# Kernel optimization log

Hardware: AMD Instinct MI355X
Metric: run time of the kernel (lower is better)

The kernel has to match this reference:

```python
import jax, jax.numpy as jnp
import numpy as np


def setup_inputs() -> dict:
    key = jax.random.key(0)
    ks = jax.random.split(key, 8)
    B, E = 1024, 8
    dims = [480, 512, 512, 311]
    inp = {
        "x": jax.random.normal(ks[0], (B, dims[0]), dtype=jnp.float32),
        "weight_blend": jax.random.uniform(ks[1], (E, B), dtype=jnp.float32),
        "w0": jax.random.normal(ks[2], (E, dims[1], dims[0]), dtype=jnp.float32) * 0.05,
        "b0": jax.random.normal(ks[3], (E, dims[1]), dtype=jnp.float32) * 0.05,
        "w1": jax.random.normal(ks[4], (E, dims[2], dims[1]), dtype=jnp.float32) * 0.05,
        "b1": jax.random.normal(ks[5], (E, dims[2]), dtype=jnp.float32) * 0.05,
        "w2": jax.random.normal(ks[6], (E, dims[3], dims[2]), dtype=jnp.float32) * 0.05,
        "b2": jax.random.normal(ks[7], (E, dims[3]), dtype=jnp.float32) * 0.05,
    }
    return inp


def _blend_layer(h, blend, w, b):
    # Original: W_b = sum_e blend[e,b] * w[e]  (materializes [B, d_out, d_in]),
    # then matmul(W_b, h) + bias_b. Fused einsum computes identical math.
    out = jnp.einsum("eb,eoi,bi->bo", blend, w, h)
    out = out + jnp.einsum("eb,eo->bo", blend, b)
    return out


def reference(x, weight_blend, w0, b0, w1, b1, w2, b2):
    # dropout layers are identity (training=False / keep_prob=1)
    h = _blend_layer(x, weight_blend, w0, b0)
    h = jax.nn.elu(h)
    h = _blend_layer(h, weight_blend, w1, b1)
    h = jax.nn.elu(h)
    h = _blend_layer(h, weight_blend, w2, b2)  # no activation on final layer
    return h
```

## Files before the change

### kernel.cpp

```cpp
#include <hip/hip_runtime.h>

typedef __attribute__((ext_vector_type(8))) short short8;
typedef __attribute__((ext_vector_type(4))) float f32x4;

__device__ __forceinline__ unsigned short f2bf(float f) {
    unsigned u = __builtin_bit_cast(unsigned, f);
    unsigned r = (u + 0x7FFFu + ((u >> 16) & 1u)) >> 16;
    return (unsigned short)r;
}
__device__ __forceinline__ float bf2f(unsigned short u) {
    unsigned v = ((unsigned)u) << 16;
    return __builtin_bit_cast(float, v);
}

__device__ __forceinline__ void gload16(const unsigned short* g, unsigned short* l) {
    __builtin_amdgcn_global_load_lds(
        (const __attribute__((address_space(1))) void*)g,
        (__attribute__((address_space(3))) void*)l,
        16, 0, 0);
}

#define WAITV(N) asm volatile("s_waitcnt vmcnt(" #N ")" ::: "memory")
#define WAITL0() asm volatile("s_waitcnt lgkmcnt(0)" ::: "memory")
#define BAR() do { asm volatile("" ::: "memory"); __builtin_amdgcn_s_barrier(); asm volatile("" ::: "memory"); } while (0)

__device__ __forceinline__ short8 lds_read_swz(const unsigned short* tile, int row, int colb) {
    int off = row * 64 + colb;
    off ^= ((off >> 7) & 7) << 4;
    return *(const short8*)((const char*)tile + off);
}

__device__ __forceinline__ void xcd_decode(int bid, int nxt, int& x, int& y, int& z) {
    int r = bid & 7, q = bid >> 3;
    y = q & 7;
    int p = (q >> 3) * 8 + r;
    x = p % nxt; z = p / nxt;
}

__device__ __forceinline__ void cvt_chunk(const float* __restrict__ src,
                                          unsigned short* __restrict__ dst, int t) {
    const float4* s4 = (const float4*)src;
    float4 a = s4[2 * t], b = s4[2 * t + 1];
    union { unsigned short u[8]; int4 v; } r;
    r.u[0] = f2bf(a.x); r.u[1] = f2bf(a.y); r.u[2] = f2bf(a.z); r.u[3] = f2bf(a.w);
    r.u[4] = f2bf(b.x); r.u[5] = f2bf(b.y); r.u[6] = f2bf(b.z); r.u[7] = f2bf(b.w);
    ((int4*)dst)[t] = r.v;
}

__device__ __forceinline__ short8 pack8(float4 a, float4 b) {
    short8 p;
    p[0] = (short)f2bf(a.x); p[1] = (short)f2bf(a.y);
    p[2] = (short)f2bf(a.z); p[3] = (short)f2bf(a.w);
    p[4] = (short)f2bf(b.x); p[5] = (short)f2bf(b.y);
    p[6] = (short)f2bf(b.z); p[7] = (short)f2bf(b.w);
    return p;
}

__global__ __launch_bounds__(512) void k_gemm0(
    const float* __restrict__ A, const float* __restrict__ W,
    const float* __restrict__ blend, const float* __restrict__ bias,
    unsigned short* __restrict__ Y,
    const float* __restrict__ csrc, unsigned short* __restrict__ cdst)
{
    __shared__ unsigned short As[2][4096];
    __shared__ unsigned short Bs[2][4096];

    int bx, by, e;
    xcd_decode(blockIdx.x, 4, bx, by, e);
    const int bm = by * 128;
    const int on = bx * 128;
    const int t  = threadIdx.x, lane = t & 63, w = t >> 6;
    const int wr = w >> 2, wc = w & 3;

    const int sr = lane >> 2, sce = (lane & 3) * 8;
    const int ra = w * 16 + sr;
    const float* gA = A + (size_t)(bm + ra) * 480 + sce;
    const float* gB = W + ((size_t)e * 512 + (on + ra)) * 480 + sce;

    int woff = ra * 64 + (lane & 3) * 16;
    woff ^= ((woff >> 7) & 7) << 4;

    float4 La0[3], La1[3], Lb0[3], Lb1[3];
    #pragma unroll
    for (int s = 0; s < 3; ++s) {
        int k0 = s * 32;
        La0[s] = *(const float4*)(gA + k0); La1[s] = *(const float4*)(gA + k0 + 4);
        Lb0[s] = *(const float4*)(gB + k0); Lb1[s] = *(const float4*)(gB + k0 + 4);
    }

    f32x4 acc[4][2] = {};

    #pragma unroll
    for (int kt = 0; kt < 15; ++kt) {
        const int s = kt % 3, buf = kt & 1;
        *(short8*)((char*)As[buf] + woff) = pack8(La0[s], La1[s]);
        *(short8*)((char*)Bs[buf] + woff) = pack8(Lb0[s], Lb1[s]);
        WAITL0();
        BAR();
        if (kt + 3 < 15) {
            int k0 = (kt + 3) * 32;
            La0[s] = *(const float4*)(gA + k0); La1[s] = *(const float4*)(gA + k0 + 4);
            Lb0[s] = *(const float4*)(gB + k0); Lb1[s] = *(const float4*)(gB + k0 + 4);
        }
        short8 af[4], bfr[2];
        #pragma unroll
        for (int fm = 0; fm < 4; ++fm)
            af[fm] = lds_read_swz(As[buf], wr * 64 + fm * 16 + (lane & 15), (lane >> 4) * 16);
        #pragma unroll
        for (int fn = 0; fn < 2; ++fn)
            bfr[fn] = lds_read_swz(Bs[buf], wc * 32 + fn * 16 + (lane & 15), (lane >> 4) * 16);
        #pragma unroll
        for (int fm = 0; fm < 4; ++fm)
            #pragma unroll
            for (int fn = 0; fn < 2; ++fn)
                acc[fm][fn] = __builtin_amdgcn_mfma_f32_16x16x32_bf16(
                    af[fm], bfr[fn], acc[fm][fn], 0, 0, 0);
    }

    const float* blendE = blend + e * 1024;
    const float* biasE  = bias + (size_t)e * 512;
    unsigned short* Ye  = Y + (size_t)e * 1024 * 512;
    #pragma unroll
    for (int fm = 0; fm < 4; ++fm) {
        int i0 = bm + wr * 64 + fm * 16 + (lane >> 4) * 4;
        float4 bl = *(const float4*)&blendE[i0];
        #pragma unroll
        for (int fn = 0; fn < 2; ++fn) {
            int j = on + wc * 32 + fn * 16 + (lane & 15);
            float bs = biasE[j];
            #pragma unroll
            for (int r = 0; r < 4; ++r)
                Ye[(size_t)(i0 + r) * 512 + j] = f2bf((acc[fm][fn][r] + bs) * ((&bl.x)[r]));
        }
    }

    int lb = (e * 8 + by) * 4 + bx;
    cvt_chunk(csrc, cdst, lb * 1024 + threadIdx.x);
    cvt_chunk(csrc, cdst, lb * 1024 + 512 + threadIdx.x);
}

__global__ __launch_bounds__(512) void k_gemm(
    const unsigned short* __restrict__ A,
    const unsigned short* __restrict__ W,
    const float* __restrict__ blend, const float* __restrict__ bias,
    unsigned short* __restrict__ Y,
    int N, int ldy, int nxt,
    const float* __restrict__ csrc, unsigned short* __restrict__ cdst, int nchunk)
{
    __shared__ unsigned short As[4][4096];
    __shared__ unsigned short Bs[4][4096];

    int bx, by, e;
    xcd_decode(blockIdx.x, nxt, bx, by, e);
    const int bm = by * 128;
    const int on = bx * 128;
    const int t  = threadIdx.x, lane = t & 63, w = t >> 6;
    const int wr = w >> 2, wc = w & 3;

    const unsigned short* Wt = W + (size_t)e * N * 512;
    const int l2 = lane ^ ((lane >> 3) & 7);
    const int sr = l2 >> 2, sce = (l2 & 3) * 8;
    const int ra = w * 16 + sr;
    int rb = on + ra; if (rb > N - 1) rb = N - 1;
    const unsigned short* gA = A  + (size_t)(bm + ra) * 512 + sce;
    const unsigned short* gB = Wt + (size_t)rb * 512 + sce;

#define STAGE(buf, kt) do { int _k0 = (kt) * 32;                       \
        gload16(gA + _k0, &As[(buf)][w * 512]);                        \
        gload16(gB + _k0, &Bs[(buf)][w * 512]); } while (0)

#define COMPUTE(cur) do {                                                          \
        short8 af[4], bfr[2];                                                      \
        _Pragma("unroll")                                                          \
        for (int fm = 0; fm < 4; ++fm)                                             \
            af[fm] = lds_read_swz(As[(cur)], wr * 64 + fm * 16 + (lane & 15), (lane >> 4) * 16); \
        _Pragma("unroll")                                                          \
        for (int fn = 0; fn < 2; ++fn)                                             \
            bfr[fn] = lds_read_swz(Bs[(cur)], wc * 32 + fn * 16 + (lane & 15), (lane >> 4) * 16); \
        _Pragma("unroll")                                                          \
        for (int fm = 0; fm < 4; ++fm)                                             \
            _Pragma("unroll")                                                      \
            for (int fn = 0; fn < 2; ++fn)                                         \
                acc[fm][fn] = __builtin_amdgcn_mfma_f32_16x16x32_bf16(             \
                    af[fm], bfr[fn], acc[fm][fn], 0, 0, 0);                        \
    } while (0)

    f32x4 acc[4][2] = {};
    STAGE(0, 0); STAGE(1, 1); STAGE(2, 2);

    for (int kt = 0; kt < 13; ++kt) {
        WAITV(4);
        BAR();
        STAGE((kt + 3) & 3, kt + 3);
        COMPUTE(kt & 3);
    }
    WAITV(4); BAR(); COMPUTE(1);
    WAITV(2); BAR(); COMPUTE(2);
    WAITV(0); BAR(); COMPUTE(3);
#undef STAGE

    const float* blendE = blend + e * 1024;
    const float* biasE  = bias + (size_t)e * N;
    unsigned short* Ye  = Y + (size_t)e * 1024 * ldy;
    #pragma unroll
    for (int fm = 0; fm < 4; ++fm) {
        int i0 = bm + wr * 64 + fm * 16 + (lane >> 4) * 4;
        float4 bl = *(const float4*)&blendE[i0];
        #pragma unroll
        for (int fn = 0; fn < 2; ++fn) {
            int j = on + wc * 32 + fn * 16 + (lane & 15);
            if (j < N) {
                float bs = biasE[j];
                #pragma unroll
                for (int r = 0; r < 4; ++r)
                    Ye[(size_t)(i0 + r) * ldy + j] = f2bf((acc[fm][fn][r] + bs) * ((&bl.x)[r]));
            }
        }
    }

    if (cdst) {
        int lb = (e * 8 + by) * nxt + bx;
        #pragma unroll
        for (int q = 0; q < 2; ++q) {
            int tl = q * 512 + threadIdx.x;
            if (tl < nchunk) cvt_chunk(csrc, cdst, lb * nchunk + tl);
        }
    }
}

__global__ __launch_bounds__(256) void k_reduce8(
    const unsigned short* __restrict__ Y, unsigned short* __restrict__ out)
{
    int idx = blockIdx.x * 256 + threadIdx.x;
    int b  = idx >> 6;
    int o0 = (idx & 63) * 8;
    size_t base = (size_t)b * 512 + o0;
    float s[8] = {};
    #pragma unroll
    for (int p = 0; p < 8; ++p) {
        int4 v = *(const int4*)&Y[base + (size_t)p * 1024 * 512];
        const unsigned short* u = (const unsigned short*)&v;
        #pragma unroll
        for (int r = 0; r < 8; ++r) s[r] += bf2f(u[r]);
    }
    union { unsigned short u[8]; int4 v; } rr;
    #pragma unroll
    for (int r = 0; r < 8; ++r) {
        float v = (s[r] > 0.f) ? s[r] : expm1f(s[r]);
        rr.u[r] = f2bf(v);
    }
    *(int4*)&out[base] = rr.v;
}

__global__ __launch_bounds__(256) void k_reduce_last(
    const unsigned short* __restrict__ Y, float* __restrict__ out)
{
    int idx = blockIdx.x * 256 + threadIdx.x;
    if (idx >= 1024 * 40) return;
    int b  = idx / 40;
    int o0 = (idx - b * 40) * 8;
    size_t base = (size_t)b * 320 + o0;
    float s[8] = {};
    #pragma unroll
    for (int p = 0; p < 8; ++p) {
        int4 v = *(const int4*)&Y[base + (size_t)p * 1024 * 320];
        const unsigned short* u = (const unsigned short*)&v;
        #pragma unroll
        for (int r = 0; r < 8; ++r) s[r] += bf2f(u[r]);
    }
    #pragma unroll
    for (int r = 0; r < 8; ++r)
        if (o0 + r < 311) out[(size_t)b * 311 + o0 + r] = s[r];
}

extern "C" void kernel_launch(void* const* d_in, const int* in_sizes, int n_in,
                              void* d_out, int out_size, void* d_ws, size_t ws_size,
                              hipStream_t stream) {
    const float* x     = (const float*)d_in[0];
    const float* blend = (const float*)d_in[1];
    const float* w0    = (const float*)d_in[2];
    const float* b0    = (const float*)d_in[3];
    const float* w1    = (const float*)d_in[4];
    const float* b1    = (const float*)d_in[5];
    const float* w2    = (const float*)d_in[6];
    const float* b2    = (const float*)d_in[7];

    char* ws = (char*)d_ws;
    unsigned short* w1b = (unsigned short*)(ws + 0);
    unsigned short* w2b = (unsigned short*)(ws + 4194304);
    unsigned short* h1b = (unsigned short*)(ws + 6742016);
    unsigned short* h2b = (unsigned short*)(ws + 7790592);
    unsigned short* yb  = (unsigned short*)(ws + 8839168);

    k_gemm0<<<256, 512, 0, stream>>>(x, w0, blend, b0, yb, w1, w1b);
    k_reduce8<<<256, 256, 0, stream>>>(yb, h1b);

    k_gemm<<<256, 512, 0, stream>>>(h1b, w1b, blend, b1, yb, 512, 512, 4,
                                    w2, w2b, 622);
    k_reduce8<<<256, 256, 0, stream>>>(yb, h2b);

    k_gemm<<<192, 512, 0, stream>>>(h2b, w2b, blend, b2, yb, 311, 320, 3,
                                    nullptr, nullptr, 0);
    k_reduce_last<<<160, 256, 0, stream>>>(yb, (float*)d_out);
}
```

Measured before the change: 53.17 us.

## Split K across two warp groups with LDS reduction in blended GEMM

The 8 waves are split into two groups that process alternating K tiles. Each wave now computes a 64x64 output subtile (4x4 MFMA fragments) instead of 64x32, which halves the LDS fragment reads per MFMA. The partial accumulators are then reduced through shared memory in two rounds before one group writes the epilogue. This doubles the accumulator registers per wave and adds extra barriers and LDS traffic for the reduction.

Result: slower. 59.48 us (+11.9%).

```diff
diff --git a/kernel.cpp b/kernel.cpp
--- a/kernel.cpp
+++ b/kernel.cpp
@@ -147,15 +147,18 @@
     int N, int ldy, int nxt,
     const float* __restrict__ csrc, unsigned short* __restrict__ cdst, int nchunk)
 {
-    __shared__ unsigned short As[4][4096];
-    __shared__ unsigned short Bs[4][4096];
+    __shared__ char smem[65536];
+    unsigned short (*As)[4096] = (unsigned short (*)[4096])smem;
+    unsigned short (*Bs)[4096] = (unsigned short (*)[4096])(smem + 32768);
 
     int bx, by, e;
     xcd_decode(blockIdx.x, nxt, bx, by, e);
     const int bm = by * 128;
     const int on = bx * 128;
     const int t  = threadIdx.x, lane = t & 63, w = t >> 6;
-    const int wr = w >> 2, wc = w & 3;
+    const int wk = w >> 2;
+    const int ws = w & 3;
+    const int wr = ws >> 1, wc = ws & 1;
 
     const unsigned short* Wt = W + (size_t)e * N * 512;
     const int l2 = lane ^ ((lane >> 3) & 7);
@@ -170,50 +173,86 @@
         gload16(gB + _k0, &Bs[(buf)][w * 512]); } while (0)
 
 #define COMPUTE(cur) do {                                                          \
-        short8 af[4], bfr[2];                                                      \
+        short8 af[4], bfr[4];                                                      \
         _Pragma("unroll")                                                          \
         for (int fm = 0; fm < 4; ++fm)                                             \
             af[fm] = lds_read_swz(As[(cur)], wr * 64 + fm * 16 + (lane & 15), (lane >> 4) * 16); \
         _Pragma("unroll")                                                          \
-        for (int fn = 0; fn < 2; ++fn)                                             \
-            bfr[fn] = lds_read_swz(Bs[(cur)], wc * 32 + fn * 16 + (lane & 15), (lane >> 4) * 16); \
+        for (int fn = 0; fn < 4; ++fn)                                             \
+            bfr[fn] = lds_read_swz(Bs[(cur)], wc * 64 + fn * 16 + (lane & 15), (lane >> 4) * 16); \
         _Pragma("unroll")                                                          \
         for (int fm = 0; fm < 4; ++fm)                                             \
             _Pragma("unroll")                                                      \
-            for (int fn = 0; fn < 2; ++fn)                                         \
+            for (int fn = 0; fn < 4; ++fn)                                         \
                 acc[fm][fn] = __builtin_amdgcn_mfma_f32_16x16x32_bf16(             \
                     af[fm], bfr[fn], acc[fm][fn], 0, 0, 0);                        \
     } while (0)
 
-    f32x4 acc[4][2] = {};
+    f32x4 acc[4][4] = {};
     STAGE(0, 0); STAGE(1, 1); STAGE(2, 2);
 
     for (int kt = 0; kt < 13; ++kt) {
         WAITV(4);
         BAR();
         STAGE((kt + 3) & 3, kt + 3);
-        COMPUTE(kt & 3);
-    }
-    WAITV(4); BAR(); COMPUTE(1);
-    WAITV(2); BAR(); COMPUTE(2);
-    WAITV(0); BAR(); COMPUTE(3);
+        if ((kt & 1) == wk) COMPUTE(kt & 3);
+    }
+    WAITV(4); BAR(); if (wk == 1) COMPUTE(1);
+    WAITV(2); BAR(); if (wk == 0) COMPUTE(2);
+    WAITV(0); BAR(); if (wk == 1) COMPUTE(3);
 #undef STAGE
 
-    const float* blendE = blend + e * 1024;
-    const float* biasE  = bias + (size_t)e * N;
-    unsigned short* Ye  = Y + (size_t)e * 1024 * ldy;
-    #pragma unroll
-    for (int fm = 0; fm < 4; ++fm) {
-        int i0 = bm + wr * 64 + fm * 16 + (lane >> 4) * 4;
-        float4 bl = *(const float4*)&blendE[i0];
-        #pragma unroll
-        for (int fn = 0; fn < 2; ++fn) {
-            int j = on + wc * 32 + fn * 16 + (lane & 15);
-            if (j < N) {
-                float bs = biasE[j];
+    float* fsc = (float*)smem;
+    #pragma unroll
+    for (int rnd = 0; rnd < 2; ++rnd) {
+        BAR();
+        if (wk == 1 && (ws >> 1) == rnd) {
+            float* base = fsc + (ws & 1) * 4096;
+            #pragma unroll
+            for (int fm = 0; fm < 4; ++fm)
                 #pragma unroll
-                for (int r = 0; r < 4; ++r)
-                    Ye[(size_t)(i0 + r) * ldy + j] = f2bf((acc[fm][fn][r] + bs) * ((&bl.x)[r]));
+                for (int fn = 0; fn < 4; ++fn)
+                    #pragma unroll
+                    for (int r = 0; r < 4; ++r) {
+                        int row = fm * 16 + (lane >> 4) * 4 + r;
+                        int col = fn * 16 + (lane & 15);
+                        base[row * 64 + col] = acc[fm][fn][r];
+                    }
+        }
+        WAITL0();
+        BAR();
+        if (wk == 0 && (ws >> 1) == rnd) {
+            float* base = fsc + (ws & 1) * 4096;
+            #pragma unroll
+            for (int fm = 0; fm < 4; ++fm)
+                #pragma unroll
+                for (int fn = 0; fn < 4; ++fn)
+                    #pragma unroll
+                    for (int r = 0; r < 4; ++r) {
+                        int row = fm * 16 + (lane >> 4) * 4 + r;
+                        int col = fn * 16 + (lane & 15);
+                        acc[fm][fn][r] += base[row * 64 + col];
+                    }
+        }
+    }
+
+    if (wk == 0) {
+        const float* blendE = blend + e * 1024;
+        const float* biasE  = bias + (size_t)e * N;
+        unsigned short* Ye  = Y + (size_t)e * 1024 * ldy;
+        #pragma unroll
+        for (int fm = 0; fm < 4; ++fm) {
+            int i0 = bm + wr * 64 + fm * 16 + (lane >> 4) * 4;
+            float4 bl = *(const float4*)&blendE[i0];
+            #pragma unroll
+            for (int fn = 0; fn < 4; ++fn) {
+                int j = on + wc * 64 + fn * 16 + (lane & 15);
+                if (j < N) {
+                    float bs = biasE[j];
+                    #pragma unroll
+                    for (int r = 0; r < 4; ++r)
+                        Ye[(size_t)(i0 + r) * ldy + j] = f2bf((acc[fm][fn][r] + bs) * ((&bl.x)[r]));
+                }
             }
         }
     }
```
